# Performance work log

Measured on AMD Instinct MI355X. Metric: run time of the kernel, lower is better.

The kernel has to match this reference:

```python
import jax, jax.numpy as jnp
import numpy as np

EPS = 1e-6
NUM_HEADS = 8
NUM_TOKENS = 196

def setup_inputs() -> dict:
    key = jax.random.key(0)
    ks = jax.random.split(key, 4)
    B, N, C = 32, 3136, 384
    H, Dh, M = NUM_HEADS, C // NUM_HEADS, NUM_TOKENS
    return {
        "x": jax.random.normal(ks[0], (B, N, C), dtype=jnp.float32),
        "q_param": jax.random.normal(ks[1], (1, M, H, Dh), dtype=jnp.float32) * 0.02,
        "kv_w": jax.random.normal(ks[2], (2 * C, C), dtype=jnp.float32) * 0.02,
        "proj_w": jax.random.normal(ks[3], (C, C), dtype=jnp.float32) * 0.02,
        "proj_b": jnp.zeros((C,), dtype=jnp.float32),
        "ln_w": jnp.ones((C,), dtype=jnp.float32),
        "ln_b": jnp.zeros((C,), dtype=jnp.float32),
    }

def reference(x, q_param, kv_w, proj_w, proj_b, ln_w, ln_b):
    B, N, C = x.shape
    H = NUM_HEADS
    Dh = C // H
    # LayerNorm (eps=1e-6)
    mu = jnp.mean(x, axis=-1, keepdims=True)
    var = jnp.mean(jnp.square(x - mu), axis=-1, keepdims=True)
    x = (x - mu) * jax.lax.rsqrt(var + EPS) * ln_w + ln_b
    # exact GELU (nn.GELU default)
    x = jax.nn.gelu(x, approximate=False)
    # kv projection (no bias): [B,N,2C] -> k,v each [B,H,N,Dh]
    kv = (x @ kv_w.T).reshape(B, N, 2, H, Dh)
    kv = jnp.transpose(kv, (2, 0, 3, 1, 4))
    k, v = kv[0], kv[1]
    # learnable queries: (1,M,H,Dh) -> (1,H,M,Dh)
    q = jnp.transpose(q_param, (0, 2, 1, 3))
    # NOTE: source applies NO 1/sqrt(Dh) scaling
    attn = jnp.einsum("bhmd,bhnd->bhmn", jnp.broadcast_to(q, (B, H, NUM_TOKENS, Dh)), k)
    attn = jax.nn.softmax(attn, axis=-1)
    out = jnp.einsum("bhmn,bhnd->bhmd", attn, v)  # [B,H,M,Dh]
    out = jnp.transpose(out, (0, 2, 1, 3)).reshape(B, NUM_TOKENS, C)
    return out @ proj_w.T + proj_b
```

## Files before the change

kernel.cpp:

```cpp
#include <hip/hip_runtime.h>
#include <stdint.h>

typedef float f32x4 __attribute__((ext_vector_type(4)));
typedef short s16x8 __attribute__((ext_vector_type(8)));
typedef short s16x4 __attribute__((ext_vector_type(4)));
typedef unsigned short ushort_t;

#define B_  32
#define N_  3136
#define C_  384
#define H_  8
#define DH_ 48
#define M_  196
#define ROWS  (B_*N_)
#define PROWS (B_*M_)

static __device__ __forceinline__ ushort_t f2bf(float f) {
  union { float f; uint32_t u; } v; v.f = f;
  uint32_t r = (v.u + 0x7fffu + ((v.u >> 16) & 1u)) >> 16;
  return (ushort_t)r;
}
static __device__ __forceinline__ ushort_t f2bf_fast(float f) {
  union { float f; uint32_t u; } v; v.f = f;
  return (ushort_t)((v.u + 0x8000u) >> 16);
}

static __device__ __forceinline__ f32x4 mfma_16x16x32(s16x8 a, s16x8 b, f32x4 c) {
  return __builtin_amdgcn_mfma_f32_16x16x32_bf16(a, b, c, 0, 0, 0);
}

static __device__ __forceinline__ f32x4 mfma_16x16x16(s16x4 a, s16x4 b, f32x4 c) {
#if __has_builtin(__builtin_amdgcn_mfma_f32_16x16x16_bf16)
  return __builtin_amdgcn_mfma_f32_16x16x16_bf16(a, b, c, 0, 0, 0);
#elif __has_builtin(__builtin_amdgcn_mfma_f32_16x16x16bf16_1k)
  return __builtin_amdgcn_mfma_f32_16x16x16bf16_1k(a, b, c, 0, 0, 0);
#else
  f32x4 d;
  asm("v_mfma_f32_16x16x16_bf16 %0, %1, %2, %3" : "=v"(d) : "v"(a), "v"(b), "v"(c));
  return d;
#endif
}

static __device__ __forceinline__ void gload_lds16(const void* g, void* l) {
  __builtin_amdgcn_global_load_lds(
      (const __attribute__((address_space(1))) void*)(uintptr_t)g,
      (__attribute__((address_space(3))) void*)(uint32_t)(uintptr_t)l,
      16, 0, 0);
}

__global__ __launch_bounds__(256) void k_ln_gelu(
    const float* __restrict__ x, const float* __restrict__ lnw,
    const float* __restrict__ lnb, ushort_t* __restrict__ x16) {
  int row = blockIdx.x * 4 + (threadIdx.x >> 6);
  int lane = threadIdx.x & 63;
  const float2* xr = (const float2*)(x + (size_t)row * C_);
  float2 v0 = xr[lane], v1 = xr[lane + 64], v2 = xr[lane + 128];
  float s  = v0.x + v0.y + v1.x + v1.y + v2.x + v2.y;
  float ss = v0.x*v0.x + v0.y*v0.y + v1.x*v1.x + v1.y*v1.y + v2.x*v2.x + v2.y*v2.y;
#pragma unroll
  for (int off = 1; off < 64; off <<= 1) {
    s  += __shfl_xor(s, off);
    ss += __shfl_xor(ss, off);
  }
  float mu = s * (1.0f / C_);
  float rs = rsqrtf(ss * (1.0f / C_) - mu * mu + 1e-6f);
  const float2* wr = (const float2*)lnw;
  const float2* br = (const float2*)lnb;
  uint32_t* outp = (uint32_t*)(x16 + (size_t)row * C_);
#pragma unroll
  for (int t = 0; t < 3; ++t) {
    int idx = lane + t * 64;
    float2 v = (t == 0) ? v0 : ((t == 1) ? v1 : v2);
    float2 w = wr[idx], bb = br[idx];
    float a0 = (v.x - mu) * rs * w.x + bb.x;
    float a1 = (v.y - mu) * rs * w.y + bb.y;
    a0 = 0.5f * a0 * (1.0f + erff(a0 * 0.70710678118654752440f));
    a1 = 0.5f * a1 * (1.0f + erff(a1 * 0.70710678118654752440f));
    outp[idx] = (uint32_t)f2bf_fast(a0) | ((uint32_t)f2bf_fast(a1) << 16);
  }
}

__global__ __launch_bounds__(256) void k_convert(
    const float* __restrict__ kvw, const float* __restrict__ pw,
    const float* __restrict__ qp, ushort_t* __restrict__ wkv16,
    ushort_t* __restrict__ wp16, ushort_t* __restrict__ q16) {
  int i = blockIdx.x * 256 + threadIdx.x;
  if (i < 2 * C_ * C_) wkv16[i] = f2bf(kvw[i]);
  if (i < C_ * C_)     wp16[i]  = f2bf(pw[i]);
  if (i < M_ * H_ * DH_) {
    int d = i % DH_; int t = i / DH_; int h = t % H_; int m = t / H_;
    q16[((size_t)h * M_ + m) * DH_ + d] = f2bf(qp[i]);
  }
}

template <typename OutT, bool BIAS, bool SWZ>
__global__ __launch_bounds__(256) void k_gemm_bt(
    const ushort_t* __restrict__ A, const ushort_t* __restrict__ Bw,
    OutT* __restrict__ Co, const float* __restrict__ bias,
    int M, int N, int K, int ntn) {
  __shared__ ushort_t lA[128 * 32];
  __shared__ ushort_t lB[128 * 32];
  int bid = blockIdx.x;
  if (SWZ) bid = (bid & 7) * (gridDim.x >> 3) + (bid >> 3);
  int tr = bid / ntn, tc = bid % ntn;
  int tid = threadIdx.x;
  int w = tid >> 6, l = tid & 63;
  int wr = w >> 1, wc = w & 1;
  int c = l & 15, g = l >> 4;
  f32x4 acc[4][4];
#pragma unroll
  for (int i = 0; i < 4; ++i)
#pragma unroll
    for (int j = 0; j < 4; ++j) acc[i][j] = (f32x4){0.f, 0.f, 0.f, 0.f};
  const size_t a0 = (size_t)tr * 128, b0 = (size_t)tc * 128;
  int srow = l >> 2;
  int scol = (l & 3) * 8;
  for (int kt = 0; kt < K; kt += 32) {
    __syncthreads();
#pragma unroll
    for (int r = 0; r < 2; ++r) {
      int lr = w * 16 + r * 64;
      gload_lds16(A  + (a0 + lr + srow) * (size_t)K + kt + scol, &lA[lr * 32]);
      gload_lds16(Bw + (b0 + lr + srow) * (size_t)K + kt + scol, &lB[lr * 32]);
    }
    __syncthreads();
    s16x8 af[4], bf[4];
#pragma unroll
    for (int i = 0; i < 4; ++i)
      af[i] = *(const s16x8*)&lA[(wr * 64 + i * 16 + c) * 32 + g * 8];
#pragma unroll
    for (int j = 0; j < 4; ++j)
      bf[j] = *(const s16x8*)&lB[(wc * 64 + j * 16 + c) * 32 + g * 8];
#pragma unroll
    for (int i = 0; i < 4; ++i)
#pragma unroll
      for (int j = 0; j < 4; ++j)
        acc[i][j] = mfma_16x16x32(bf[j], af[i], acc[i][j]);
  }
  int g4 = g * 4;
#pragma unroll
  for (int i = 0; i < 4; ++i) {
    size_t row = a0 + wr * 64 + i * 16 + c;
#pragma unroll
    for (int j = 0; j < 4; ++j) {
      size_t colb = b0 + wc * 64 + j * 16 + g4;
      if constexpr (sizeof(OutT) == 2) {
        uint2 val;
        val.x = (uint32_t)f2bf_fast(acc[i][j][0]) | ((uint32_t)f2bf_fast(acc[i][j][1]) << 16);
        val.y = (uint32_t)f2bf_fast(acc[i][j][2]) | ((uint32_t)f2bf_fast(acc[i][j][3]) << 16);
        *(uint2*)&Co[row * N + colb] = val;
      } else {
        float4 val;
        if constexpr (BIAS) {
          float4 bs = *(const float4*)&bias[colb];
          val.x = acc[i][j][0] + bs.x; val.y = acc[i][j][1] + bs.y;
          val.z = acc[i][j][2] + bs.z; val.w = acc[i][j][3] + bs.w;
        } else {
          val.x = acc[i][j][0]; val.y = acc[i][j][1];
          val.z = acc[i][j][2]; val.w = acc[i][j][3];
        }
        *(float4*)&Co[row * N + colb] = val;
      }
    }
  }
}

__global__ __launch_bounds__(512) void k_attn(
    const ushort_t* __restrict__ kv, const ushort_t* __restrict__ q16,
    ushort_t* __restrict__ att16) {
  int b = blockIdx.x >> 3, h = blockIdx.x & 7;
  __shared__ ushort_t Kl[64 * 72];
  __shared__ ushort_t Vt[48 * 76];
  int tid = threadIdx.x;
  int w = tid >> 6, l = tid & 63;
  int c = l & 15, g = l >> 4;
  for (int i = tid; i < 64 * 72; i += 512) Kl[i] = 0;
  for (int i = tid; i < 48 * 76; i += 512) Vt[i] = 0;
  s16x8 qf[2][2];
#pragma unroll
  for (int i = 0; i < 2; ++i)
#pragma unroll
    for (int kk = 0; kk < 2; ++kk) {
      int m = w * 32 + i * 16 + c;
      int dh = kk * 32 + g * 8;
      s16x8 z = {0, 0, 0, 0, 0, 0, 0, 0};
      qf[i][kk] = (m < M_ && dh < DH_)
                      ? *(const s16x8*)(q16 + ((size_t)h * M_ + m) * DH_ + dh)
                      : z;
    }
  f32x4 o[3][2];
#pragma unroll
  for (int f = 0; f < 3; ++f)
#pragma unroll
    for (int i = 0; i < 2; ++i) o[f][i] = (f32x4){0.f, 0.f, 0.f, 0.f};
  float rm[2] = {-3e38f, -3e38f}, rl[2] = {0.f, 0.f};
  int srow = tid >> 3, spart = tid & 7;
  const size_t rowstride = (size_t)(2 * C_);
  uint32_t kr0, kr1, kr2, vr0, vr1, vr2;
  {
    size_t gb = ((size_t)b * N_ + srow) * rowstride + h * DH_ + spart * 6;
    kr0 = *(const uint32_t*)(kv + gb);
    kr1 = *(const uint32_t*)(kv + gb + 2);
    kr2 = *(const uint32_t*)(kv + gb + 4);
    vr0 = *(const uint32_t*)(kv + gb + C_);
    vr1 = *(const uint32_t*)(kv + gb + C_ + 2);
    vr2 = *(const uint32_t*)(kv + gb + C_ + 4);
  }
  __syncthreads();

  for (int t = 0; t < 49; ++t) {
    uint32_t* kd = (uint32_t*)&Kl[srow * 72 + spart * 6];
    kd[0] = kr0; kd[1] = kr1; kd[2] = kr2;
    int dbase = spart * 6;
    Vt[(dbase + 0) * 76 + srow] = (ushort_t)vr0;
    Vt[(dbase + 1) * 76 + srow] = (ushort_t)(vr0 >> 16);
    Vt[(dbase + 2) * 76 + srow] = (ushort_t)vr1;
    Vt[(dbase + 3) * 76 + srow] = (ushort_t)(vr1 >> 16);
    Vt[(dbase + 4) * 76 + srow] = (ushort_t)vr2;
    Vt[(dbase + 5) * 76 + srow] = (ushort_t)(vr2 >> 16);
    __syncthreads();
    {
      int tn = (t < 48) ? t + 1 : t;
      size_t gb = ((size_t)b * N_ + tn * 64 + srow) * rowstride + h * DH_ + spart * 6;
      kr0 = *(const uint32_t*)(kv + gb);
      kr1 = *(const uint32_t*)(kv + gb + 2);
      kr2 = *(const uint32_t*)(kv + gb + 4);
      vr0 = *(const uint32_t*)(kv + gb + C_);
      vr1 = *(const uint32_t*)(kv + gb + C_ + 2);
      vr2 = *(const uint32_t*)(kv + gb + C_ + 4);
    }
    f32x4 s[4][2];
#pragma unroll
    for (int j = 0; j < 4; ++j) {
      s16x8 kf0 = *(const s16x8*)&Kl[(j * 16 + c) * 72 + g * 8];
      s16x8 kf1 = *(const s16x8*)&Kl[(j * 16 + c) * 72 + 32 + g * 8];
#pragma unroll
      for (int i = 0; i < 2; ++i) {
        f32x4 z = {0.f, 0.f, 0.f, 0.f};
        f32x4 t0 = mfma_16x16x32(kf0, qf[i][0], z);
        s[j][i] = mfma_16x16x32(kf1, qf[i][1], t0);
      }
    }
    s16x4 pb[2][4];
#pragma unroll
    for (int i = 0; i < 2; ++i) {
      float tm = s[0][i][0];
#pragma unroll
      for (int j = 0; j < 4; ++j)
#pragma unroll
        for (int q = 0; q < 4; ++q) tm = fmaxf(tm, s[j][i][q]);
      tm = fmaxf(tm, __shfl_xor(tm, 16));
      tm = fmaxf(tm, __shfl_xor(tm, 32));
      float nm = fmaxf(rm[i], tm);
      float corr = __expf(rm[i] - nm);
      rm[i] = nm;
      float ts = 0.f;
#pragma unroll
      for (int j = 0; j < 4; ++j) {
        float p0 = __expf(s[j][i][0] - nm);
        float p1 = __expf(s[j][i][1] - nm);
        float p2 = __expf(s[j][i][2] - nm);
        float p3 = __expf(s[j][i][3] - nm);
        ts += (p0 + p1) + (p2 + p3);
        pb[i][j] = (s16x4){(short)f2bf_fast(p0), (short)f2bf_fast(p1),
                           (short)f2bf_fast(p2), (short)f2bf_fast(p3)};
      }
      ts += __shfl_xor(ts, 16);
      ts += __shfl_xor(ts, 32);
      rl[i] = rl[i] * corr + ts;
#pragma unroll
      for (int f = 0; f < 3; ++f) o[f][i] *= corr;
    }
#pragma unroll
    for (int f = 0; f < 3; ++f)
#pragma unroll
      for (int j = 0; j < 4; ++j) {
        s16x4 vf = *(const s16x4*)&Vt[(f * 16 + c) * 76 + j * 16 + g * 4];
        o[f][0] = mfma_16x16x16(vf, pb[0][j], o[f][0]);
        o[f][1] = mfma_16x16x16(vf, pb[1][j], o[f][1]);
      }
    __syncthreads();
  }
#pragma unroll
  for (int i = 0; i < 2; ++i) {
    int m = w * 32 + i * 16 + c;
    if (m < M_) {
      float inv = 1.0f / rl[i];
#pragma unroll
      for (int f = 0; f < 3; ++f) {
        uint32_t w0 = (uint32_t)f2bf_fast(o[f][i][0] * inv) |
                      ((uint32_t)f2bf_fast(o[f][i][1] * inv) << 16);
        uint32_t w1 = (uint32_t)f2bf_fast(o[f][i][2] * inv) |
                      ((uint32_t)f2bf_fast(o[f][i][3] * inv) << 16);
        uint2 val; val.x = w0; val.y = w1;
        *(uint2*)&att16[((size_t)b * M_ + m) * C_ + h * DH_ + f * 16 + g * 4] = val;
      }
    }
  }
}

extern "C" void kernel_launch(void* const* d_in, const int* in_sizes, int n_in,
                              void* d_out, int out_size, void* d_ws, size_t ws_size,
                              hipStream_t stream) {
  (void)in_sizes; (void)n_in; (void)out_size; (void)ws_size;
  const float* x   = (const float*)d_in[0];
  const float* qp  = (const float*)d_in[1];
  const float* kvw = (const float*)d_in[2];
  const float* pw  = (const float*)d_in[3];
  const float* pbv = (const float*)d_in[4];
  const float* lnw = (const float*)d_in[5];
  const float* lnb = (const float*)d_in[6];
  float* out = (float*)d_out;

  ushort_t* x16   = (ushort_t*)d_ws;
  ushort_t* kv16  = x16 + (size_t)ROWS * C_;
  ushort_t* att16 = kv16 + (size_t)ROWS * 2 * C_;
  ushort_t* wkv16 = att16 + (size_t)PROWS * C_;
  ushort_t* wp16  = wkv16 + 2 * C_ * C_;
  ushort_t* q16   = wp16 + C_ * C_;

  hipLaunchKernelGGL(k_ln_gelu, dim3(ROWS / 4), dim3(256), 0, stream, x, lnw, lnb, x16);
  hipLaunchKernelGGL(k_convert, dim3((2 * C_ * C_ + 255) / 256), dim3(256), 0, stream,
                     kvw, pw, qp, wkv16, wp16, q16);
  hipLaunchKernelGGL((k_gemm_bt<ushort_t, false, true>),
                     dim3((ROWS / 128) * (2 * C_ / 128)), dim3(256), 0, stream,
                     x16, wkv16, kv16, (const float*)nullptr, ROWS, 2 * C_, C_, 2 * C_ / 128);
  hipLaunchKernelGGL(k_attn, dim3(B_ * H_), dim3(512), 0, stream, kv16, q16, att16);
  hipLaunchKernelGGL((k_gemm_bt<float, true, false>),
                     dim3((PROWS / 128) * (C_ / 128)), dim3(256), 0, stream,
                     att16, wp16, out, pbv, PROWS, C_, C_, C_ / 128);
}
```

Before: 288.2 us.

## Double-buffer LDS tiles in GEMM and rework epilogue to per-column stores

```diff
diff --git a/kernel.cpp b/kernel.cpp
--- a/kernel.cpp
+++ b/kernel.cpp
@@ -98,8 +98,8 @@
     const ushort_t* __restrict__ A, const ushort_t* __restrict__ Bw,
     OutT* __restrict__ Co, const float* __restrict__ bias,
     int M, int N, int K, int ntn) {
-  __shared__ ushort_t lA[128 * 32];
-  __shared__ ushort_t lB[128 * 32];
+  __shared__ ushort_t lA[2][128 * 32];
+  __shared__ ushort_t lB[2][128 * 32];
   int bid = blockIdx.x;
   if (SWZ) bid = (bid & 7) * (gridDim.x >> 3) + (bid >> 3);
   int tr = bid / ntn, tc = bid % ntn;
@@ -115,51 +115,51 @@
   const size_t a0 = (size_t)tr * 128, b0 = (size_t)tc * 128;
   int srow = l >> 2;
   int scol = (l & 3) * 8;
-  for (int kt = 0; kt < K; kt += 32) {
+#pragma unroll
+  for (int r = 0; r < 2; ++r) {
+    int lr = w * 16 + r * 64;
+    gload_lds16(A  + (a0 + lr + srow) * (size_t)K + scol, &lA[0][lr * 32]);
+    gload_lds16(Bw + (b0 + lr + srow) * (size_t)K + scol, &lB[0][lr * 32]);
+  }
+  __syncthreads();
+  const int T = K >> 5;
+  for (int t = 0; t < T; ++t) {
+    int cur = t & 1;
+    if (t + 1 < T) {
+      int kt = (t + 1) << 5;
+#pragma unroll
+      for (int r = 0; r < 2; ++r) {
+        int lr = w * 16 + r * 64;
+        gload_lds16(A  + (a0 + lr + srow) * (size_t)K + kt + scol, &lA[cur ^ 1][lr * 32]);
+        gload_lds16(Bw + (b0 + lr + srow) * (size_t)K + kt + scol, &lB[cur ^ 1][lr * 32]);
+      }
+    }
+    s16x8 af[4], bf[4];
+#pragma unroll
+    for (int i = 0; i < 4; ++i)
+      af[i] = *(const s16x8*)&lA[cur][(wr * 64 + i * 16 + c) * 32 + g * 8];
+#pragma unroll
+    for (int j = 0; j < 4; ++j)
+      bf[j] = *(const s16x8*)&lB[cur][(wc * 64 + j * 16 + c) * 32 + g * 8];
+#pragma unroll
+    for (int i = 0; i < 4; ++i)
+#pragma unroll
+      for (int j = 0; j < 4; ++j)
+        acc[i][j] = mfma_16x16x32(af[i], bf[j], acc[i][j]);
     __syncthreads();
-#pragma unroll
-    for (int r = 0; r < 2; ++r) {
-      int lr = w * 16 + r * 64;
-      gload_lds16(A  + (a0 + lr + srow) * (size_t)K + kt + scol, &lA[lr * 32]);
-      gload_lds16(Bw + (b0 + lr + srow) * (size_t)K + kt + scol, &lB[lr * 32]);
-    }
-    __syncthreads();
-    s16x8 af[4], bf[4];
-#pragma unroll
-    for (int i = 0; i < 4; ++i)
-      af[i] = *(const s16x8*)&lA[(wr * 64 + i * 16 + c) * 32 + g * 8];
-#pragma unroll
-    for (int j = 0; j < 4; ++j)
-      bf[j] = *(const s16x8*)&lB[(wc * 64 + j * 16 + c) * 32 + g * 8];
-#pragma unroll
-    for (int i = 0; i < 4; ++i)
-#pragma unroll
-      for (int j = 0; j < 4; ++j)
-        acc[i][j] = mfma_16x16x32(bf[j], af[i], acc[i][j]);
-  }
-  int g4 = g * 4;
+  }
 #pragma unroll
   for (int i = 0; i < 4; ++i) {
-    size_t row = a0 + wr * 64 + i * 16 + c;
 #pragma unroll
     for (int j = 0; j < 4; ++j) {
-      size_t colb = b0 + wc * 64 + j * 16 + g4;
-      if constexpr (sizeof(OutT) == 2) {
-        uint2 val;
-        val.x = (uint32_t)f2bf_fast(acc[i][j][0]) | ((uint32_t)f2bf_fast(acc[i][j][1]) << 16);
-        val.y = (uint32_t)f2bf_fast(acc[i][j][2]) | ((uint32_t)f2bf_fast(acc[i][j][3]) << 16);
-        *(uint2*)&Co[row * N + colb] = val;
-      } else {
-        float4 val;
-        if constexpr (BIAS) {
-          float4 bs = *(const float4*)&bias[colb];
-          val.x = acc[i][j][0] + bs.x; val.y = acc[i][j][1] + bs.y;
-          val.z = acc[i][j][2] + bs.z; val.w = acc[i][j][3] + bs.w;
-        } else {
-          val.x = acc[i][j][0]; val.y = acc[i][j][1];
-          val.z = acc[i][j][2]; val.w = acc[i][j][3];
-        }
-        *(float4*)&Co[row * N + colb] = val;
+      size_t col = b0 + wc * 64 + j * 16 + c;
+      float bs = BIAS ? bias[col] : 0.0f;
+#pragma unroll
+      for (int q = 0; q < 4; ++q) {
+        size_t row = a0 + wr * 64 + i * 16 + g * 4 + q;
+        float v = acc[i][j][q] + bs;
+        if constexpr (sizeof(OutT) == 2) Co[row * N + col] = f2bf(v);
+        else                             Co[row * N + col] = v;
       }
     }
   }
```

After: 265.3 us. 7.9% less time.
